# Kernel optimization log

Measured on AMD Instinct MI355X. Metric: run time of the kernel, lower is better.

The kernel has to match this reference:

```python
import jax, jax.numpy as jnp
import numpy as np

ALPHA = 0.1        # dt / tau = 1 / 10
SIGMA_REC = 0.03
SIGMA_INP = 0.03


def setup_inputs() -> dict:
    key = jax.random.key(0)
    ks = jax.random.split(key, 7)
    n, N, num_inputs, num_outputs, T, B = 128, 1024, 6, 2, 512, 256
    u = jax.random.normal(ks[0], (num_inputs, T, B), dtype=jnp.float32)
    rec_noise = jax.random.normal(ks[1], (B, T, n), dtype=jnp.float32)
    inp_noise = jax.random.normal(ks[2], (B, T, num_inputs), dtype=jnp.float32)
    W_inp = jax.random.normal(ks[3], (n, num_inputs), dtype=jnp.float32) / np.float32(np.sqrt(num_inputs))
    # spectral-ish scaling keeps the leaky RNN stable over 512 steps
    W_rec = jax.random.normal(ks[4], (n, n), dtype=jnp.float32) * np.float32(0.9 / np.sqrt(n))
    W_out = jax.random.normal(ks[5], (num_outputs, n), dtype=jnp.float32) / np.float32(np.sqrt(n))
    # q is orthonormalized via SVD in the torch module (make_orthonormal)
    q0 = np.asarray(jax.random.uniform(ks[6], (n, N)), dtype=np.float32)
    U, _, Vh = np.linalg.svd(q0, full_matrices=False)
    q = jnp.asarray((U @ Vh).astype(np.float32))
    return dict(u=u, rec_noise=rec_noise, inp_noise=inp_noise,
                W_inp=W_inp, W_rec=W_rec, W_out=W_out, q=q)


def reference(u, rec_noise, inp_noise, W_inp, W_rec, W_out, q):
    # u: (num_inputs, T, B); noise tensors already batch-major (B, T, .)
    B = u.shape[-1]
    n = W_rec.shape[0]
    rn = jnp.sqrt(2.0 / ALPHA * SIGMA_REC ** 2) * rec_noise      # (B, T, n)
    inoise = jnp.sqrt(2.0 / ALPHA * SIGMA_INP ** 2) * inp_noise  # (B, T, num_inputs)
    ub = jnp.swapaxes(u, 0, -1)                                  # (B, T, num_inputs)
    x0 = jnp.zeros((B, n), dtype=u.dtype)                        # initial state self.x = 0

    def step(x, ins):
        u_t, in_t, rn_t = ins
        x_new = (1.0 - ALPHA) * x + ALPHA * (
            jax.nn.relu(x @ W_rec.T + (u_t + in_t) @ W_inp.T) + rn_t)
        return x_new, x_new

    # T-1 update steps using inputs at t = 0 .. T-2 (matches the torch loop)
    xs_in = (jnp.swapaxes(ub, 0, 1)[:-1],
             jnp.swapaxes(inoise, 0, 1)[:-1],
             jnp.swapaxes(rn, 0, 1)[:-1])
    _, xs = jax.lax.scan(step, x0, xs_in)                        # (T-1, B, n)
    states = jnp.concatenate([x0[:, None, :], jnp.swapaxes(xs, 0, 1)], axis=1)  # (B, T, n)

    outputs = jnp.swapaxes(states @ W_out.T, 0, -1)              # (num_outputs, T, B)
    states_embedded = jnp.swapaxes(states @ q, 0, -1)            # (N, T, B)
    return states_embedded, outputs
```

## Files before the change

### kernel.cpp

```cpp
#include <hip/hip_runtime.h>
#include <hip/hip_bf16.h>

#define T_STEPS 512
#define BATCH   256
#define NN      128
#define NEMB    1024
#define M_ROWS  (T_STEPS * BATCH)
#define NOISE_K 0.13416407864998738f
#define CH      8
#define NCHUNK  (T_STEPS / CH)

typedef short s16x8 __attribute__((ext_vector_type(8)));
typedef float f32x4 __attribute__((ext_vector_type(4)));

__device__ __forceinline__ unsigned short f2bf(float f) {
  union { float f; unsigned u; } v; v.f = f;
  unsigned r = v.u + 0x7fffu + ((v.u >> 16) & 1u);
  return (unsigned short)(r >> 16);
}
__device__ __forceinline__ float bf2f(unsigned short s) {
  union { unsigned u; float f; } v; v.u = ((unsigned)s) << 16;
  return v.f;
}

__global__ __launch_bounds__(256) void rnn_step_kernel(
    const float* __restrict__ u,
    const float* __restrict__ rec_noise,
    const float* __restrict__ inp_noise,
    const float* __restrict__ W_inp,
    const float* __restrict__ W_rec,
    unsigned short* __restrict__ states)
{
  const int b   = blockIdx.x;
  const int tid = threadIdx.x;
  const int i   = tid >> 1;
  const int h   = tid & 1;

  __shared__ float xbuf[2][136];
  __shared__ float rns[2][CH * NN];
  __shared__ float us[2][CH][8];

  float4 w[16];
  {
    const float4* wr = (const float4*)(W_rec + i * NN + h * 64);
    #pragma unroll
    for (int c = 0; c < 16; ++c) w[c] = wr[c];
  }
  float winp[6];
  #pragma unroll
  for (int j = 0; j < 6; ++j) winp[j] = W_inp[i * 6 + j];

  const int ts6 = tid / 6, j6 = tid - ts6 * 6;

  if (tid < 136) xbuf[0][tid] = 0.f;
  if (h == 0) states[b * NN + i] = 0;

  {
    const f32x4* src = (const f32x4*)(rec_noise + (size_t)b * T_STEPS * NN);
    *(f32x4*)&rns[0][tid * 4] = src[tid];
    if (tid < 48) {
      float uu = u[j6 * (T_STEPS * BATCH) + ts6 * BATCH + b];
      float in = inp_noise[((size_t)b * T_STEPS + ts6) * 6 + j6];
      us[0][ts6][j6] = uu + NOISE_K * in;
    }
  }
  __syncthreads();

  float xr = 0.f;
  for (int c = 0; c < NCHUNK; ++c) {
    const int cb = c & 1;

    f32x4 rn_pf = {0.f, 0.f, 0.f, 0.f};
    float u_pf = 0.f, in_pf = 0.f;
    if (c < NCHUNK - 1) {
      const f32x4* src =
          (const f32x4*)(rec_noise + ((size_t)b * T_STEPS + (c + 1) * CH) * NN);
      rn_pf = src[tid];
      if (tid < 48) {
        const int tt = (c + 1) * CH + ts6;
        u_pf  = u[j6 * (T_STEPS * BATCH) + tt * BATCH + b];
        in_pf = inp_noise[((size_t)b * T_STEPS + tt) * 6 + j6];
      }
    }

    #pragma unroll
    for (int ts = 0; ts < CH; ++ts) {
      const int t = c * CH + ts;
      if (t > T_STEPS - 2) break;
      const int cur = ts & 1, nxt = cur ^ 1;

      const float* xb = &xbuf[cur][h * 68];
      float a0 = 0.f, a1 = 0.f, a2 = 0.f, a3 = 0.f;
      #pragma unroll
      for (int cc = 0; cc < 16; cc += 4) {
        float4 v0 = *(const float4*)&xb[(cc + 0) * 4];
        float4 v1 = *(const float4*)&xb[(cc + 1) * 4];
        float4 v2 = *(const float4*)&xb[(cc + 2) * 4];
        float4 v3 = *(const float4*)&xb[(cc + 3) * 4];
        a0 = fmaf(w[cc+0].x, v0.x, a0); a0 = fmaf(w[cc+0].y, v0.y, a0);
        a0 = fmaf(w[cc+0].z, v0.z, a0); a0 = fmaf(w[cc+0].w, v0.w, a0);
        a1 = fmaf(w[cc+1].x, v1.x, a1); a1 = fmaf(w[cc+1].y, v1.y, a1);
        a1 = fmaf(w[cc+1].z, v1.z, a1); a1 = fmaf(w[cc+1].w, v1.w, a1);
        a2 = fmaf(w[cc+2].x, v2.x, a2); a2 = fmaf(w[cc+2].y, v2.y, a2);
        a2 = fmaf(w[cc+2].z, v2.z, a2); a2 = fmaf(w[cc+2].w, v2.w, a2);
        a3 = fmaf(w[cc+3].x, v3.x, a3); a3 = fmaf(w[cc+3].y, v3.y, a3);
        a3 = fmaf(w[cc+3].z, v3.z, a3); a3 = fmaf(w[cc+3].w, v3.w, a3);
      }
      float acc = (a0 + a1) + (a2 + a3);
      acc += __shfl_xor(acc, 1);

      float inp = 0.f;
      #pragma unroll
      for (int j = 0; j < 6; ++j) inp = fmaf(winp[j], us[cb][ts][j], inp);

      const float pre = acc + inp;
      const float r   = pre > 0.f ? pre : 0.f;
      const float xn  = 0.9f * xr + 0.1f * (r + NOISE_K * rns[cb][ts * NN + i]);
      xr = xn;

      if (h == 0) {
        xbuf[nxt][i + ((i >> 6) << 2)] = xn;
        states[((t + 1) * BATCH + b) * NN + i] = f2bf(xn);
      }
      __syncthreads();
    }

    if (c < NCHUNK - 1) {
      *(f32x4*)&rns[cb ^ 1][tid * 4] = rn_pf;
      if (tid < 48) us[cb ^ 1][ts6][j6] = u_pf + NOISE_K * in_pf;
      __syncthreads();
    }
  }
}

__global__ __launch_bounds__(256) void emb_kernel(
    const unsigned short* __restrict__ states,
    const float* __restrict__ q,
    float* __restrict__ out)
{
  const int jt  = blockIdx.x;
  const int mt  = blockIdx.y;
  const int tid = threadIdx.x;
  const int w   = tid >> 6;
  const int l   = tid & 63;
  const int lg  = l >> 4;
  const int lr  = l & 15;

  __shared__ unsigned short qt[64 * 128];

  {
    const int j  = tid & 63;
    const int k0 = tid >> 6;
    #pragma unroll
    for (int kk = k0; kk < 128; kk += 4) {
      float v = q[kk * NEMB + jt * 64 + j];
      int k8 = kk >> 3, e = kk & 7;
      qt[j * 128 + ((k8 ^ (j & 7)) << 3) + e] = f2bf(v);
    }
  }

  s16x8 afrag[2][4];
  #pragma unroll
  for (int mf = 0; mf < 2; ++mf) {
    const int m = mt * 128 + w * 32 + mf * 16 + lr;
    const unsigned short* arow = states + m * NN;
    #pragma unroll
    for (int kc = 0; kc < 4; ++kc)
      afrag[mf][kc] = *(const s16x8*)(arow + kc * 32 + lg * 8);
  }
  __syncthreads();

  f32x4 acc[2][4] = {};
  #pragma unroll
  for (int kc = 0; kc < 4; ++kc) {
    s16x8 bfrag[4];
    #pragma unroll
    for (int jf = 0; jf < 4; ++jf) {
      const int jl = jf * 16 + lr;
      bfrag[jf] = *(const s16x8*)(qt + jl * 128 + ((((kc << 2) + lg) ^ (jl & 7)) << 3));
    }
    #pragma unroll
    for (int mf = 0; mf < 2; ++mf)
      #pragma unroll
      for (int jf = 0; jf < 4; ++jf)
        acc[mf][jf] = __builtin_amdgcn_mfma_f32_16x16x32_bf16(
            afrag[mf][kc], bfrag[jf], acc[mf][jf], 0, 0, 0);
  }

  #pragma unroll
  for (int mf = 0; mf < 2; ++mf) {
    const int m = mt * 128 + w * 32 + mf * 16 + lg * 4;
    #pragma unroll
    for (int jf = 0; jf < 4; ++jf) {
      const long j = jt * 64 + jf * 16 + lr;
      *(f32x4*)&out[j * M_ROWS + m] = acc[mf][jf];
    }
  }
}

__global__ __launch_bounds__(256) void wout_kernel(
    const unsigned short* __restrict__ states,
    const float* __restrict__ W_out,
    float* __restrict__ out)
{
  __shared__ float wo[2 * NN];
  const int tid = threadIdx.x;
  wo[tid] = W_out[tid];
  __syncthreads();

  const int m = blockIdx.x * 256 + tid;
  const unsigned short* row = states + (size_t)m * NN;
  float a0 = 0.f, a1 = 0.f;
  #pragma unroll
  for (int c = 0; c < 16; ++c) {
    s16x8 v = *(const s16x8*)(row + c * 8);
    #pragma unroll
    for (int e = 0; e < 8; ++e) {
      float x = bf2f((unsigned short)v[e]);
      a0 = fmaf(x, wo[c * 8 + e], a0);
      a1 = fmaf(x, wo[NN + c * 8 + e], a1);
    }
  }
  out[(long)1024 * M_ROWS + m] = a0;
  out[(long)1025 * M_ROWS + m] = a1;
}

extern "C" void kernel_launch(void* const* d_in, const int* in_sizes, int n_in,
                              void* d_out, int out_size, void* d_ws, size_t ws_size,
                              hipStream_t stream) {
  const float* u         = (const float*)d_in[0];
  const float* rec_noise = (const float*)d_in[1];
  const float* inp_noise = (const float*)d_in[2];
  const float* W_inp     = (const float*)d_in[3];
  const float* W_rec     = (const float*)d_in[4];
  const float* W_out     = (const float*)d_in[5];
  const float* q         = (const float*)d_in[6];
  float* out = (float*)d_out;
  unsigned short* states = (unsigned short*)d_ws;

  rnn_step_kernel<<<dim3(BATCH), dim3(256), 0, stream>>>(
      u, rec_noise, inp_noise, W_inp, W_rec, states);

  dim3 g2(NEMB / 64, M_ROWS / 128);
  emb_kernel<<<g2, dim3(256), 0, stream>>>(states, q, out);

  wout_kernel<<<dim3(M_ROWS / 256), dim3(256), 0, stream>>>(states, W_out, out);
}
```

Baseline: 470.5 us.

## Fuse W_out projection into embedding kernel and stage output stores through LDS

Removes the separate wout kernel. Blocks with jt==0 now compute the two output projections from the bf16 state fragments they already hold in registers. The embedding epilogue writes accumulators into a padded shared tile and then stores full 512-byte contiguous rows, replacing the scattered 16-byte stores. The RNN kernel also gets launch_bounds(256,1) and scalarized W_rec registers to avoid spilling or scratch indexing. The cost is extra LDS per block (about 34KB for the transpose tile), which may lower occupancy, plus divergent extra work in the jt==0 blocks.

```diff
diff --git a/kernel.cpp b/kernel.cpp
--- a/kernel.cpp
+++ b/kernel.cpp
@@ -23,7 +23,7 @@
   return v.f;
 }
 
-__global__ __launch_bounds__(256) void rnn_step_kernel(
+__global__ __launch_bounds__(256, 1) void rnn_step_kernel(
     const float* __restrict__ u,
     const float* __restrict__ rec_noise,
     const float* __restrict__ inp_noise,
@@ -40,12 +40,12 @@
   __shared__ float rns[2][CH * NN];
   __shared__ float us[2][CH][8];
 
-  float4 w[16];
-  {
-    const float4* wr = (const float4*)(W_rec + i * NN + h * 64);
-    #pragma unroll
-    for (int c = 0; c < 16; ++c) w[c] = wr[c];
-  }
+  const float4* wr = (const float4*)(W_rec + i * NN + h * 64);
+  const float4 w0 = wr[0],  w1 = wr[1],  w2 = wr[2],  w3 = wr[3];
+  const float4 w4 = wr[4],  w5 = wr[5],  w6 = wr[6],  w7 = wr[7];
+  const float4 w8 = wr[8],  w9 = wr[9],  wA = wr[10], wB = wr[11];
+  const float4 wC = wr[12], wD = wr[13], wE = wr[14], wF = wr[15];
+
   float winp[6];
   #pragma unroll
   for (int j = 0; j < 6; ++j) winp[j] = W_inp[i * 6 + j];
@@ -91,21 +91,15 @@
 
       const float* xb = &xbuf[cur][h * 68];
       float a0 = 0.f, a1 = 0.f, a2 = 0.f, a3 = 0.f;
-      #pragma unroll
-      for (int cc = 0; cc < 16; cc += 4) {
-        float4 v0 = *(const float4*)&xb[(cc + 0) * 4];
-        float4 v1 = *(const float4*)&xb[(cc + 1) * 4];
-        float4 v2 = *(const float4*)&xb[(cc + 2) * 4];
-        float4 v3 = *(const float4*)&xb[(cc + 3) * 4];
-        a0 = fmaf(w[cc+0].x, v0.x, a0); a0 = fmaf(w[cc+0].y, v0.y, a0);
-        a0 = fmaf(w[cc+0].z, v0.z, a0); a0 = fmaf(w[cc+0].w, v0.w, a0);
-        a1 = fmaf(w[cc+1].x, v1.x, a1); a1 = fmaf(w[cc+1].y, v1.y, a1);
-        a1 = fmaf(w[cc+1].z, v1.z, a1); a1 = fmaf(w[cc+1].w, v1.w, a1);
-        a2 = fmaf(w[cc+2].x, v2.x, a2); a2 = fmaf(w[cc+2].y, v2.y, a2);
-        a2 = fmaf(w[cc+2].z, v2.z, a2); a2 = fmaf(w[cc+2].w, v2.w, a2);
-        a3 = fmaf(w[cc+3].x, v3.x, a3); a3 = fmaf(w[cc+3].y, v3.y, a3);
-        a3 = fmaf(w[cc+3].z, v3.z, a3); a3 = fmaf(w[cc+3].w, v3.w, a3);
-      }
+      #define STEP4(W, IDX, ACC)                                  \
+        { float4 xv = *(const float4*)&xb[(IDX) * 4];             \
+          ACC = fmaf(W.x, xv.x, ACC); ACC = fmaf(W.y, xv.y, ACC); \
+          ACC = fmaf(W.z, xv.z, ACC); ACC = fmaf(W.w, xv.w, ACC); }
+      STEP4(w0, 0, a0) STEP4(w1, 1, a1) STEP4(w2, 2, a2) STEP4(w3, 3, a3)
+      STEP4(w4, 4, a0) STEP4(w5, 5, a1) STEP4(w6, 6, a2) STEP4(w7, 7, a3)
+      STEP4(w8, 8, a0) STEP4(w9, 9, a1) STEP4(wA, 10, a2) STEP4(wB, 11, a3)
+      STEP4(wC, 12, a0) STEP4(wD, 13, a1) STEP4(wE, 14, a2) STEP4(wF, 15, a3)
+      #undef STEP4
       float acc = (a0 + a1) + (a2 + a3);
       acc += __shfl_xor(acc, 1);
 
@@ -136,6 +130,7 @@
 __global__ __launch_bounds__(256) void emb_kernel(
     const unsigned short* __restrict__ states,
     const float* __restrict__ q,
+    const float* __restrict__ W_out,
     float* __restrict__ out)
 {
   const int jt  = blockIdx.x;
@@ -147,6 +142,8 @@
   const int lr  = l & 15;
 
   __shared__ unsigned short qt[64 * 128];
+  __shared__ float tr[64 * 132];
+  __shared__ float wos[2 * NN];
 
   {
     const int j  = tid & 63;
@@ -158,6 +155,7 @@
       qt[j * 128 + ((k8 ^ (j & 7)) << 3) + e] = f2bf(v);
     }
   }
+  if (jt == 0) wos[tid] = W_out[tid];
 
   s16x8 afrag[2][4];
   #pragma unroll
@@ -187,42 +185,47 @@
             afrag[mf][kc], bfrag[jf], acc[mf][jf], 0, 0, 0);
   }
 
+  if (jt == 0) {
+    #pragma unroll
+    for (int mf = 0; mf < 2; ++mf) {
+      float s0 = 0.f, s1 = 0.f;
+      #pragma unroll
+      for (int kc = 0; kc < 4; ++kc) {
+        const int kb = kc * 32 + lg * 8;
+        const s16x8 af = afrag[mf][kc];
+        #pragma unroll
+        for (int e = 0; e < 8; ++e) {
+          const float x = bf2f((unsigned short)af[e]);
+          s0 = fmaf(x, wos[kb + e], s0);
+          s1 = fmaf(x, wos[NN + kb + e], s1);
+        }
+      }
+      s0 += __shfl_xor(s0, 16); s0 += __shfl_xor(s0, 32);
+      s1 += __shfl_xor(s1, 16); s1 += __shfl_xor(s1, 32);
+      if (lg == 0) {
+        const long m = (long)mt * 128 + w * 32 + mf * 16 + lr;
+        out[(long)1024 * M_ROWS + m] = s0;
+        out[(long)1025 * M_ROWS + m] = s1;
+      }
+    }
+  }
+
   #pragma unroll
   for (int mf = 0; mf < 2; ++mf) {
-    const int m = mt * 128 + w * 32 + mf * 16 + lg * 4;
-    #pragma unroll
-    for (int jf = 0; jf < 4; ++jf) {
-      const long j = jt * 64 + jf * 16 + lr;
-      *(f32x4*)&out[j * M_ROWS + m] = acc[mf][jf];
-    }
-  }
-}
-
-__global__ __launch_bounds__(256) void wout_kernel(
-    const unsigned short* __restrict__ states,
-    const float* __restrict__ W_out,
-    float* __restrict__ out)
-{
-  __shared__ float wo[2 * NN];
-  const int tid = threadIdx.x;
-  wo[tid] = W_out[tid];
+    const int m0 = w * 32 + mf * 16 + lg * 4;
+    #pragma unroll
+    for (int jf = 0; jf < 4; ++jf)
+      *(f32x4*)&tr[(jf * 16 + lr) * 132 + m0] = acc[mf][jf];
+  }
   __syncthreads();
 
-  const int m = blockIdx.x * 256 + tid;
-  const unsigned short* row = states + (size_t)m * NN;
-  float a0 = 0.f, a1 = 0.f;
-  #pragma unroll
-  for (int c = 0; c < 16; ++c) {
-    s16x8 v = *(const s16x8*)(row + c * 8);
-    #pragma unroll
-    for (int e = 0; e < 8; ++e) {
-      float x = bf2f((unsigned short)v[e]);
-      a0 = fmaf(x, wo[c * 8 + e], a0);
-      a1 = fmaf(x, wo[NN + c * 8 + e], a1);
-    }
-  }
-  out[(long)1024 * M_ROWS + m] = a0;
-  out[(long)1025 * M_ROWS + m] = a1;
+  const int mo = (tid & 31) * 4;
+  #pragma unroll
+  for (int p = 0; p < 8; ++p) {
+    const int jr = p * 8 + (tid >> 5);
+    f32x4 v = *(const f32x4*)&tr[jr * 132 + mo];
+    *(f32x4*)&out[(long)(jt * 64 + jr) * M_ROWS + mt * 128 + mo] = v;
+  }
 }
 
 extern "C" void kernel_launch(void* const* d_in, const int* in_sizes, int n_in,
@@ -242,7 +245,5 @@
       u, rec_noise, inp_noise, W_inp, W_rec, states);
 
   dim3 g2(NEMB / 64, M_ROWS / 128);
-  emb_kernel<<<g2, dim3(256), 0, stream>>>(states, q, out);
-
-  wout_kernel<<<dim3(M_ROWS / 256), dim3(256), 0, stream>>>(states, W_out, out);
-}
+  emb_kernel<<<g2, dim3(256), 0, stream>>>(states, q, W_out, out);
+}
```

After: 457.5 us. -2.8%, faster.
